# Performance work log

Hardware: AMD Instinct MI355X
Metric: run time of the kernel (lower is better)

Reference implementation:

```python
import jax, jax.numpy as jnp
import numpy as np

L, C, K, V, G, T, NC, CIN = 9, 256, 3, 25, 9, 128, 60, 3


def _ln(x, w, b, axes, eps=1e-5):
    # LayerNorm over (channels, joints) per time step, affine params broadcast over time
    m = x.mean(axes, keepdims=True)
    v = x.var(axes, keepdims=True)
    return (x - m) * jax.lax.rsqrt(v + eps) * w + b


def setup_inputs() -> dict:
    key = jax.random.key(0)
    ks = jax.random.split(key, 8)
    s = 0.02  # weight init scale
    return {
        "x": jax.random.normal(ks[0], (1, CIN, T, V), jnp.float32),
        "A": jax.random.uniform(ks[1], (K, V, V), jnp.float32),
        "ln_in_w": jnp.ones((CIN, V), jnp.float32),
        "ln_in_b": jnp.zeros((CIN, V), jnp.float32),
        "W_in": jax.random.normal(ks[2], (C, CIN), jnp.float32) * s,
        "b_in": jnp.zeros((C,), jnp.float32),
        "Wg": jax.random.normal(ks[3], (L, K * C, C), jnp.float32) * s,
        "bg": jnp.zeros((L, K * C), jnp.float32),
        "ln1_w": jnp.ones((L, C, V), jnp.float32),
        "ln1_b": jnp.zeros((L, C, V), jnp.float32),
        "Wt": jax.random.normal(ks[4], (L, C, C, G), jnp.float32) * s,
        "bt": jnp.zeros((L, C), jnp.float32),
        "ln2_w": jnp.ones((L, C, V), jnp.float32),
        "ln2_b": jnp.zeros((L, C, V), jnp.float32),
        "imp": jnp.ones((L, K, V, V), jnp.float32),
        "W_out": jax.random.normal(ks[5], (NC, C), jnp.float32) * s,
        "b_out": jnp.zeros((NC,), jnp.float32),
    }


def reference(x, A, ln_in_w, ln_in_b, W_in, b_in, Wg, bg, ln1_w, ln1_b,
              Wt, bt, ln2_w, ln2_b, imp, W_out, b_out):
    ghalf = G // 2
    Al = A[None] * imp                      # (L, K, V, V) edge-importance weighted adjacency
    xs = x[0].transpose(1, 0, 2)            # (T, CIN, V): stream frames
    fifo0 = jnp.zeros((L, C, G, V), x.dtype)

    def step(carry, xt):
        fifo, fifo_res = carry
        # input LayerNorm + 1x1 conv (fcn_in)
        h = _ln(xt, ln_in_w, ln_in_b, (0, 1))
        h = jnp.einsum('oc,cv->ov', W_in, h) + b_in[:, None]   # (C, V)
        new_f, new_fr = [], []
        for l in range(L):
            res = h                                             # identity residual (in==out, stride==1)
            # graph conv: 1x1 conv -> (K, C, V), einsum with partitioned adjacency
            y = (jnp.einsum('oc,cv->ov', Wg[l], h) + bg[l][:, None]).reshape(K, C, V)
            z = jnp.einsum('kcv,kvw->cw', y, Al[l])             # (C, V)
            # FIFO shift: newest frame at time index 0
            f = jnp.concatenate([z[:, None, :], fifo[l, :, :-1]], axis=1)      # (C, G, V)
            fr = jnp.concatenate([res[:, None, :], fifo_res[l, :, :-1]], axis=1)
            # tcn: LN -> ReLU -> temporal conv (G,1) -> LN
            a = jax.nn.relu(_ln(f, ln1_w[l][:, None, :], ln1_b[l][:, None, :], (0, 2)))
            t = jnp.einsum('ocg,cgv->ov', Wt[l], a) + bt[l][:, None]           # (C, V)
            t = _ln(t, ln2_w[l], ln2_b[l], (0, 1))
            # residual from center of residual FIFO, then ReLU
            h = jax.nn.relu(t + fr[:, ghalf])
            new_f.append(f)
            new_fr.append(fr)
        pooled = h.mean(axis=1)                                 # avg_pool2d over (T=1, V)
        logits = W_out @ pooled + b_out                         # (NC,)
        return (jnp.stack(new_f), jnp.stack(new_fr)), logits

    _, out = jax.lax.scan(step, (fifo0, fifo0), xs)
    return out  # (T, NC): per-frame class logits
```

## Files before the change

kernel.cpp:

```cpp
#include <hip/hip_runtime.h>

#define TT  128
#define CC  256
#define VV  25
#define KK  3
#define GG  9
#define LL  9
#define NCC 60
#define CINN 3
#define TV    (TT*VV)
#define N4    4096
#define KDIM2 (CC*GG)
#define UR    ((TT+8)*32)
#define KSPLIT 4
#define KCH   (KDIM2/KSPLIT)

typedef __attribute__((ext_vector_type(8))) short bf16x8;
typedef __attribute__((ext_vector_type(4))) float f32x4;
typedef unsigned short us16;

__device__ __forceinline__ us16 f2bf(float f) {
    union { float f; unsigned u; } a; a.f = f;
    unsigned r = a.u + 0x7fff + ((a.u >> 16) & 1);
    return (us16)(r >> 16);
}
__device__ __forceinline__ bf16x8 ld8(const us16* p) { return *(const bf16x8*)p; }


#define PN1 (LL*KK*CC*CC)
#define PN2 (LL*CC*CC*GG)
#define PN3 (LL*KK*32*32)
#define PN4 (LL*CC*32)
#define PTOT (PN1+PN2+PN3+PN4)

__global__ void k_prep(const float* __restrict__ Wg, const float* __restrict__ Wt,
                       const float* __restrict__ A, const float* __restrict__ imp,
                       const float* __restrict__ bg,
                       us16* __restrict__ Wgb, us16* __restrict__ Wt2b,
                       us16* __restrict__ AlTb, float* __restrict__ bgAl) {
    int i = blockIdx.x * 256 + threadIdx.x;
    if (i < PN1) {
        Wgb[i] = f2bf(Wg[i]);
    } else if (i < PN1 + PN2) {
        int j = i - PN1;
        int kk = j % (CC*GG);
        int o  = (j / (CC*GG)) % CC;
        int l  = j / (CC*CC*GG);
        int g = kk >> 8, c = kk & 255;
        Wt2b[j] = f2bf(Wt[((size_t)(l*CC + o)*CC + c)*GG + g]);
    } else if (i < PN1 + PN2 + PN3) {
        int j = i - PN1 - PN2;
        int v = j & 31, w = (j >> 5) & 31;
        int lk = j >> 10, k = lk % KK, l = lk / KK;
        float val = 0.f;
        if (v < VV && w < VV)
            val = A[(k*VV+v)*VV + w] * imp[((size_t)(l*KK+k)*VV+v)*VV + w];
        AlTb[j] = f2bf(val);
    } else if (i < PTOT) {
        int j = i - PN1 - PN2 - PN3;
        int w = j & 31, c = (j >> 5) & 255, l = j >> 13;
        float s = 0.f;
        if (w < VV) {
            for (int k = 0; k < KK; k++) {
                float col = 0.f;
                for (int v = 0; v < VV; v++)
                    col += A[(k*VV+v)*VV + w] * imp[((size_t)(l*KK+k)*VV+v)*VV + w];
                s += bg[l*KK*CC + k*CC + c] * col;
            }
        }
        bgAl[j] = s;
    }
}


__global__ __launch_bounds__(256) void k_h0(const float* __restrict__ x,
                                            const float* __restrict__ lnw,
                                            const float* __restrict__ lnb,
                                            const float* __restrict__ Win,
                                            const float* __restrict__ bin,
                                            float* __restrict__ H,
                                            us16* __restrict__ Hbt2) {
    int t = blockIdx.x, tid = threadIdx.x;
    __shared__ float sx[CINN*VV];
    __shared__ float sh[CINN*VV];
    if (tid < CINN*VV)
        sx[tid] = x[(size_t)(tid/VV)*TV + t*VV + (tid%VV)];
    __syncthreads();
    float s = 0.f, q = 0.f;
    for (int i = 0; i < CINN*VV; i++) { float v = sx[i]; s += v; q += v*v; }
    float m  = s * (1.f/75.f);
    float var = q * (1.f/75.f) - m*m;
    float rs = rsqrtf(var + 1e-5f);
    if (tid < CINN*VV)
        sh[tid] = (sx[tid]-m)*rs*lnw[tid] + lnb[tid];
    __syncthreads();
    int c = tid;
    float w0 = Win[c*3+0], w1 = Win[c*3+1], w2 = Win[c*3+2], b = bin[c];
    #pragma unroll
    for (int v = 0; v < VV; v++) {
        float acc = b + w0*sh[v] + w1*sh[VV+v] + w2*sh[2*VV+v];
        H[(size_t)c*N4 + t*32 + v] = acc;
        Hbt2[(size_t)(t*32 + v)*CC + c] = f2bf(acc);
    }
    #pragma unroll
    for (int v = VV; v < 32; v++)
        Hbt2[(size_t)(t*32 + v)*CC + c] = 0;
}


__device__ __forceinline__ void blk_reduce2(float& s, float& q, float* red) {
    #pragma unroll
    for (int off = 32; off; off >>= 1) {
        s += __shfl_down(s, off);
        q += __shfl_down(q, off);
    }
    int lane = threadIdx.x & 63, w = threadIdx.x >> 6;
    if (lane == 0) { red[w] = s; red[4+w] = q; }
    __syncthreads();
    s = red[0]+red[1]+red[2]+red[3];
    q = red[4]+red[5]+red[6]+red[7];
}


__global__ __launch_bounds__(256) void k_gemm1(const us16* __restrict__ A,
                                               const us16* __restrict__ Bt,
                                               us16* __restrict__ Ybt) {
    __shared__ us16 Yl[64*72];
    const int tid = threadIdx.x;
    const int wave = tid >> 6, lane = tid & 63, quad = lane >> 4, l16 = lane & 15;
    const int m0w = blockIdx.y * 64 + (wave & 1) * 32;
    const int n0w = blockIdx.x * 64 + (wave >> 1) * 32;
    const us16* ap = A + (size_t)(m0w + l16) * CC + quad * 8;
    const us16* bp = Bt + (size_t)(n0w + l16) * CC + quad * 8;
    f32x4 acc[2][2] = {};
    #pragma unroll
    for (int s = 0; s < 8; s++) {
        bf16x8 a0 = ld8(ap + s*32);
        bf16x8 a1 = ld8(ap + s*32 + 16*CC);
        bf16x8 b0 = ld8(bp + s*32);
        bf16x8 b1 = ld8(bp + s*32 + 16*CC);
        acc[0][0] = __builtin_amdgcn_mfma_f32_16x16x32_bf16(a0, b0, acc[0][0], 0,0,0);
        acc[0][1] = __builtin_amdgcn_mfma_f32_16x16x32_bf16(a0, b1, acc[0][1], 0,0,0);
        acc[1][0] = __builtin_amdgcn_mfma_f32_16x16x32_bf16(a1, b0, acc[1][0], 0,0,0);
        acc[1][1] = __builtin_amdgcn_mfma_f32_16x16x32_bf16(a1, b1, acc[1][1], 0,0,0);
    }
    #pragma unroll
    for (int mt = 0; mt < 2; mt++)
        #pragma unroll
        for (int nt = 0; nt < 2; nt++)
            #pragma unroll
            for (int r = 0; r < 4; r++) {
                int m_loc = (wave & 1)*32 + mt*16 + quad*4 + r;
                int n_loc = (wave >> 1)*32 + nt*16 + l16;
                Yl[m_loc*72 + n_loc] = f2bf(acc[mt][nt][r]);
            }
    __syncthreads();
    const int kidx = (blockIdx.y * 64) >> 8;
    const int c0   = (blockIdx.y * 64) & 255;
    const int t0   = blockIdx.x * 2;
    #pragma unroll
    for (int u = 0; u < 2; u++) {
        int q = tid*2 + u;
        int ch = q & 3, row = q >> 2;
        int cl = row & 63, tl = row >> 6;
        bf16x8 val = *(const bf16x8*)(Yl + cl*72 + tl*32 + ch*8);
        *(bf16x8*)(Ybt + ((size_t)((t0+tl)*CC + c0 + cl))*96 + kidx*32 + ch*8) = val;
    }
}


__global__ __launch_bounds__(256) void k_adj(const us16* __restrict__ Ybt,
                                             const us16* __restrict__ AlTb,
                                             const float* __restrict__ bgAl,
                                             const float* __restrict__ lnw,
                                             const float* __restrict__ lnb,
                                             us16* __restrict__ Ut2) {
    int t = blockIdx.x, tid = threadIdx.x;
    if (t >= TT) {
        int tp = t - TT, c = tid;
        #pragma unroll
        for (int w = 0; w < 32; w++) {
            float u = (w < VV) ? fmaxf(lnb[c*VV + w], 0.f) : 0.f;
            Ut2[(size_t)(tp*32 + w)*CC + c] = f2bf(u);
        }
        return;
    }
    __shared__ float red[8];
    const int wave = tid >> 6, lane = tid & 63, quad = lane >> 4, l16 = lane & 15;
    bf16x8 al[2][3];
    #pragma unroll
    for (int nt = 0; nt < 2; nt++)
        #pragma unroll
        for (int s = 0; s < 3; s++)
            al[nt][s] = ld8(AlTb + (size_t)(s*32 + nt*16 + l16)*32 + quad*8);
    f32x4 z[4][2];
    #pragma unroll
    for (int mt = 0; mt < 4; mt++) { z[mt][0] = (f32x4){}; z[mt][1] = (f32x4){}; }
    #pragma unroll
    for (int mt = 0; mt < 4; mt++) {
        const us16* yp = Ybt + ((size_t)(t*CC + wave*64 + mt*16 + l16))*96 + quad*8;
        #pragma unroll
        for (int s = 0; s < 3; s++) {
            bf16x8 a = ld8(yp + s*32);
            z[mt][0] = __builtin_amdgcn_mfma_f32_16x16x32_bf16(a, al[0][s], z[mt][0], 0,0,0);
            z[mt][1] = __builtin_amdgcn_mfma_f32_16x16x32_bf16(a, al[1][s], z[mt][1], 0,0,0);
        }
    }
    float s_ = 0.f, q_ = 0.f;
    #pragma unroll
    for (int mt = 0; mt < 4; mt++)
        #pragma unroll
        for (int nt = 0; nt < 2; nt++)
            #pragma unroll
            for (int r = 0; r < 4; r++) {
                int c = wave*64 + mt*16 + quad*4 + r;
                int w = nt*16 + l16;
                float zb = z[mt][nt][r] + bgAl[c*32 + w];
                z[mt][nt][r] = zb;
                if (w < VV) { s_ += zb; q_ += zb*zb; }
            }
    blk_reduce2(s_, q_, red);
    float m = s_ * (1.f/6400.f);
    float var = q_ * (1.f/6400.f) - m*m;
    float rs = rsqrtf(var + 1e-5f);
    #pragma unroll
    for (int mt = 0; mt < 4; mt++)
        #pragma unroll
        for (int nt = 0; nt < 2; nt++) {
            int w = nt*16 + l16;
            if (w < VV) {
                int c0 = wave*64 + mt*16 + quad*4;
                ushort4 pk;
                float u0 = fmaxf((z[mt][nt][0]-m)*rs*lnw[(c0+0)*VV+w] + lnb[(c0+0)*VV+w], 0.f);
                float u1 = fmaxf((z[mt][nt][1]-m)*rs*lnw[(c0+1)*VV+w] + lnb[(c0+1)*VV+w], 0.f);
                float u2 = fmaxf((z[mt][nt][2]-m)*rs*lnw[(c0+2)*VV+w] + lnb[(c0+2)*VV+w], 0.f);
                float u3 = fmaxf((z[mt][nt][3]-m)*rs*lnw[(c0+3)*VV+w] + lnb[(c0+3)*VV+w], 0.f);
                pk.x = f2bf(u0); pk.y = f2bf(u1); pk.z = f2bf(u2); pk.w = f2bf(u3);
                *(ushort4*)(Ut2 + (size_t)((t+8)*32 + w)*CC + c0) = pk;
            }
        }
    #pragma unroll
    for (int r = VV; r < 32; r++)
        Ut2[(size_t)((t+8)*32 + r)*CC + tid] = 0;
}


__global__ __launch_bounds__(256) void k_gemm2(const us16* __restrict__ A,
                                               const us16* __restrict__ Ut2,
                                               float* __restrict__ TCp) {
    const int tid = threadIdx.x;
    const int wave = tid >> 6, lane = tid & 63, quad = lane >> 4, l16 = lane & 15;
    const int m0w = blockIdx.y * 64 + (wave & 1) * 32;
    const int n0w = blockIdx.x * 64 + (wave >> 1) * 32;
    const int ks = blockIdx.z;
    const int kbeg = ks * KCH, kend = kbeg + KCH;
    float* TC = TCp + (size_t)ks * CC * N4;
    const us16* ap = A + (size_t)(m0w + l16) * KDIM2 + quad * 8;
    f32x4 acc00 = {}, acc01 = {}, acc10 = {}, acc11 = {};
    bf16x8 a0, a1, b0, b1;

    auto loadAB = [&](int k0, bf16x8& x0, bf16x8& x1, bf16x8& y0, bf16x8& y1) {
        x0 = ld8(ap + k0);
        x1 = ld8(ap + k0 + 16*KDIM2);
        int g = k0 >> 8;
        const us16* bp = Ut2 + (size_t)(n0w + (8-g)*32 + l16)*CC + (k0 & 255) + quad*8;
        y0 = ld8(bp);
        y1 = ld8(bp + 16*CC);
    };
    loadAB(kbeg, a0, a1, b0, b1);
    #pragma unroll 3
    for (int k0 = kbeg + 32; k0 < kend; k0 += 32) {
        bf16x8 c0, c1, d0, d1;
        loadAB(k0, c0, c1, d0, d1);
        acc00 = __builtin_amdgcn_mfma_f32_16x16x32_bf16(a0, b0, acc00, 0,0,0);
        acc01 = __builtin_amdgcn_mfma_f32_16x16x32_bf16(a0, b1, acc01, 0,0,0);
        acc10 = __builtin_amdgcn_mfma_f32_16x16x32_bf16(a1, b0, acc10, 0,0,0);
        acc11 = __builtin_amdgcn_mfma_f32_16x16x32_bf16(a1, b1, acc11, 0,0,0);
        a0 = c0; a1 = c1; b0 = d0; b1 = d1;
    }
    acc00 = __builtin_amdgcn_mfma_f32_16x16x32_bf16(a0, b0, acc00, 0,0,0);
    acc01 = __builtin_amdgcn_mfma_f32_16x16x32_bf16(a0, b1, acc01, 0,0,0);
    acc10 = __builtin_amdgcn_mfma_f32_16x16x32_bf16(a1, b0, acc10, 0,0,0);
    acc11 = __builtin_amdgcn_mfma_f32_16x16x32_bf16(a1, b1, acc11, 0,0,0);

    const int r0 = m0w + quad*4;
    const int col = n0w + l16;
    #pragma unroll
    for (int r = 0; r < 4; r++) {
        TC[(size_t)(r0 + r)*N4 + col]           = acc00[r];
        TC[(size_t)(r0 + r)*N4 + col + 16]      = acc01[r];
        TC[(size_t)(r0 + 16 + r)*N4 + col]      = acc10[r];
        TC[(size_t)(r0 + 16 + r)*N4 + col + 16] = acc11[r];
    }
}


__global__ __launch_bounds__(256) void k_ln2(const float* __restrict__ TCp,
                                             const float* __restrict__ bt,
                                             const float* __restrict__ lnw,
                                             const float* __restrict__ lnb,
                                             const float* __restrict__ Hin,
                                             float* __restrict__ Hout,
                                             us16* __restrict__ Hbt2) {
    int t = blockIdx.x, tid = threadIdx.x;
    __shared__ float sv[CC*33];
    __shared__ float red[8];
    #pragma unroll
    for (int j = 0; j < 8; j++) {
        int c = j*32 + (tid >> 3);
        int v4 = (tid & 7) * 4;
        size_t base = (size_t)c*N4 + t*32 + v4;
        float4 x = *(const float4*)(TCp + base);
        #pragma unroll
        for (int s = 1; s < KSPLIT; s++) {
            float4 y = *(const float4*)(TCp + (size_t)s*CC*N4 + base);
            x.x += y.x; x.y += y.y; x.z += y.z; x.w += y.w;
        }
        sv[c*33 + v4+0] = x.x; sv[c*33 + v4+1] = x.y;
        sv[c*33 + v4+2] = x.z; sv[c*33 + v4+3] = x.w;
    }
    __syncthreads();
    int c = tid;
    float btc = bt[c];
    float vals[VV];
    float s = 0.f, q = 0.f;
    #pragma unroll
    for (int v = 0; v < VV; v++) {
        float x = sv[c*33 + v] + btc;
        vals[v] = x; s += x; q += x*x;
    }
    blk_reduce2(s, q, red);
    float m = s * (1.f/6400.f);
    float var = q * (1.f/6400.f) - m*m;
    float rs = rsqrtf(var + 1e-5f);
    #pragma unroll
    for (int v = 0; v < VV; v++) {
        float res = (t >= 4) ? Hin[(size_t)c*N4 + (t-4)*32 + v] : 0.f;
        float o = fmaxf((vals[v]-m)*rs*lnw[c*VV+v] + lnb[c*VV+v] + res, 0.f);
        Hout[(size_t)c*N4 + t*32 + v] = o;
        sv[c*33 + v] = o;
    }
    #pragma unroll
    for (int v = 0; v < VV; v++)
        Hbt2[(size_t)(t*32 + v)*CC + tid] = f2bf(sv[tid*33 + v]);
    #pragma unroll
    for (int v = VV; v < 32; v++)
        Hbt2[(size_t)(t*32 + v)*CC + tid] = 0;
}


__global__ __launch_bounds__(256) void k_out(const float* __restrict__ H,
                                             const float* __restrict__ Wout,
                                             const float* __restrict__ bout,
                                             float* __restrict__ out) {
    int t = blockIdx.x, tid = threadIdx.x;
    __shared__ float sp[CC];
    float s = 0.f;
    for (int v = 0; v < VV; v++) s += H[(size_t)tid*N4 + t*32 + v];
    sp[tid] = s * (1.f/VV);
    __syncthreads();
    if (tid < NCC) {
        float acc = bout[tid];
        for (int c = 0; c < CC; c++) acc = fmaf(Wout[tid*CC+c], sp[c], acc);
        out[t*NCC + tid] = acc;
    }
}


extern "C" void kernel_launch(void* const* d_in, const int* in_sizes, int n_in,
                              void* d_out, int out_size, void* d_ws, size_t ws_size,
                              hipStream_t stream) {
    const float* x    = (const float*)d_in[0];
    const float* A    = (const float*)d_in[1];
    const float* lniw = (const float*)d_in[2];
    const float* lnib = (const float*)d_in[3];
    const float* Win  = (const float*)d_in[4];
    const float* bin  = (const float*)d_in[5];
    const float* Wg   = (const float*)d_in[6];
    const float* bg   = (const float*)d_in[7];
    const float* ln1w = (const float*)d_in[8];
    const float* ln1b = (const float*)d_in[9];
    const float* Wt   = (const float*)d_in[10];
    const float* bt   = (const float*)d_in[11];
    const float* ln2w = (const float*)d_in[12];
    const float* ln2b = (const float*)d_in[13];
    const float* imp  = (const float*)d_in[14];
    const float* Wout = (const float*)d_in[15];
    const float* bout = (const float*)d_in[16];
    float* out = (float*)d_out;

    float* ws = (float*)d_ws;
    size_t off = 0;
    auto alloc = [&](size_t n) { float* p = ws + off; off += (n + 255) & ~(size_t)255; return p; };
    float* H0   = alloc((size_t)CC*N4);
    float* H1   = alloc((size_t)CC*N4);
    float* TCp  = alloc((size_t)KSPLIT*CC*N4);
    float* bgAl = alloc((size_t)LL*CC*32);
    us16* Wgb  = (us16*)alloc((size_t)LL*KK*CC*CC/2);
    us16* Wt2b = (us16*)alloc((size_t)LL*CC*KDIM2/2);
    us16* Hbt2 = (us16*)alloc((size_t)N4*CC/2);
    us16* Ut2  = (us16*)alloc((size_t)UR*CC/2);
    us16* AlTb = (us16*)alloc((size_t)LL*KK*32*32/2);
    us16* Ybt  = (us16*)alloc((size_t)TT*CC*96/2);
    (void)ws_size; (void)in_sizes; (void)n_in; (void)out_size;

    k_prep<<<(PTOT + 255)/256, 256, 0, stream>>>(Wg, Wt, A, imp, bg,
                                                 Wgb, Wt2b, AlTb, bgAl);
    k_h0<<<TT, 256, 0, stream>>>(x, lniw, lnib, Win, bin, H0, Hbt2);

    float* Hin = H0; float* Hout = H1;
    for (int l = 0; l < LL; l++) {
        k_gemm1<<<dim3(N4/64, (KK*CC)/64), 256, 0, stream>>>(
            Wgb + (size_t)l*KK*CC*CC, Hbt2, Ybt);
        k_adj<<<TT + 8, 256, 0, stream>>>(
            Ybt, AlTb + (size_t)l*KK*32*32, bgAl + (size_t)l*CC*32,
            ln1w + l*CC*VV, ln1b + l*CC*VV, Ut2);
        k_gemm2<<<dim3(N4/64, CC/64, KSPLIT), 256, 0, stream>>>(
            Wt2b + (size_t)l*CC*KDIM2, Ut2, TCp);
        k_ln2<<<TT, 256, 0, stream>>>(
            TCp, bt + l*CC, ln2w + l*CC*VV, ln2b + l*CC*VV, Hin, Hout, Hbt2);
        float* tmp = Hin; Hin = Hout; Hout = tmp;
    }
    k_out<<<TT, 256, 0, stream>>>(Hin, Wout, bout, out);
}
```

Baseline: 880.2 us.

## Fuse LN2/residual into next layer's GEMM1, drop split-K in GEMM2

Removes the separate k_ln2 kernel. Each k_gemm1 block (except layer 0) now recomputes the LayerNorm, residual add and ReLU for its two frames from the full-K GEMM2 output and stages the bf16 result in LDS as the B operand. The final layer's LN2 is folded into k_out. GEMM2 drops its 4-way split-K and uses a two-deep register prefetch instead. H is stored transposed (time-major) for coalesced residual reads. The trade-off is that all 12 row-blocks redundantly recompute the LN for their frames, and GEMM2 has 4x fewer blocks, which lowers its parallelism.

```diff
diff --git a/kernel.cpp b/kernel.cpp
--- a/kernel.cpp
+++ b/kernel.cpp
@@ -12,8 +12,8 @@
 #define N4    4096
 #define KDIM2 (CC*GG)
 #define UR    ((TT+8)*32)
-#define KSPLIT 4
-#define KCH   (KDIM2/KSPLIT)
+#define BSTR  264
+#define FSTR  33
 
 typedef __attribute__((ext_vector_type(8))) short bf16x8;
 typedef __attribute__((ext_vector_type(4))) float f32x4;
@@ -78,7 +78,7 @@
                                             const float* __restrict__ lnb,
                                             const float* __restrict__ Win,
                                             const float* __restrict__ bin,
-                                            float* __restrict__ H,
+                                            float* __restrict__ HT,
                                             us16* __restrict__ Hbt2) {
     int t = blockIdx.x, tid = threadIdx.x;
     __shared__ float sx[CINN*VV];
@@ -99,7 +99,7 @@
     #pragma unroll
     for (int v = 0; v < VV; v++) {
         float acc = b + w0*sh[v] + w1*sh[VV+v] + w2*sh[2*VV+v];
-        H[(size_t)c*N4 + t*32 + v] = acc;
+        HT[(size_t)(t*32 + v)*CC + c] = acc;
         Hbt2[(size_t)(t*32 + v)*CC + c] = f2bf(acc);
     }
     #pragma unroll
@@ -122,28 +122,97 @@
 }
 
 
+template<int FLN>
 __global__ __launch_bounds__(256) void k_gemm1(const us16* __restrict__ A,
                                                const us16* __restrict__ Bt,
+                                               const float* __restrict__ TC,
+                                               const float* __restrict__ HprevT,
+                                               const float* __restrict__ lnw,
+                                               const float* __restrict__ lnb,
+                                               const float* __restrict__ btv,
+                                               float* __restrict__ HnextT,
                                                us16* __restrict__ Ybt) {
-    __shared__ us16 Yl[64*72];
+    __shared__ __align__(16) float sF[CC*FSTR];
+    __shared__ __align__(16) us16 sB[64*BSTR];
+    __shared__ float red[8];
     const int tid = threadIdx.x;
     const int wave = tid >> 6, lane = tid & 63, quad = lane >> 4, l16 = lane & 15;
-    const int m0w = blockIdx.y * 64 + (wave & 1) * 32;
-    const int n0w = blockIdx.x * 64 + (wave >> 1) * 32;
-    const us16* ap = A + (size_t)(m0w + l16) * CC + quad * 8;
-    const us16* bp = Bt + (size_t)(n0w + l16) * CC + quad * 8;
+    const int bx = blockIdx.x, by = blockIdx.y;
+
+    if (FLN) {
+        const int t0 = bx*2;
+        const int c = tid;
+        const float btc = btv[c];
+        #pragma unroll
+        for (int f = 0; f < 2; f++) {
+            const int t = t0 + f;
+            #pragma unroll
+            for (int j = 0; j < 8; j++) {
+                int cs = j*32 + (tid >> 3);
+                int v4 = (tid & 7) * 4;
+                float4 xv = *(const float4*)(TC + (size_t)cs*N4 + t*32 + v4);
+                sF[cs*FSTR + v4+0] = xv.x; sF[cs*FSTR + v4+1] = xv.y;
+                sF[cs*FSTR + v4+2] = xv.z; sF[cs*FSTR + v4+3] = xv.w;
+            }
+            __syncthreads();
+            float vals[VV];
+            float s = 0.f, q = 0.f;
+            #pragma unroll
+            for (int v = 0; v < VV; v++) {
+                float xv = sF[c*FSTR + v] + btc;
+                vals[v] = xv; s += xv; q += xv*xv;
+            }
+            blk_reduce2(s, q, red);
+            float m = s * (1.f/6400.f);
+            float var = q * (1.f/6400.f) - m*m;
+            float rs = rsqrtf(var + 1e-5f);
+            #pragma unroll
+            for (int v = 0; v < VV; v++) {
+                float res = (t >= 4) ? HprevT[(size_t)((t-4)*32 + v)*CC + c] : 0.f;
+                float o = fmaxf((vals[v]-m)*rs*lnw[c*VV+v] + lnb[c*VV+v] + res, 0.f);
+                if (by == 0) HnextT[(size_t)(t*32 + v)*CC + c] = o;
+                sB[(f*32 + v)*BSTR + c] = f2bf(o);
+            }
+            #pragma unroll
+            for (int v = VV; v < 32; v++)
+                sB[(f*32 + v)*BSTR + c] = 0;
+            __syncthreads();
+        }
+    }
+
+    const int m0w = by*64 + (wave & 1)*32;
+    const us16* ap = A + (size_t)(m0w + l16)*CC + quad*8;
     f32x4 acc[2][2] = {};
-    #pragma unroll
-    for (int s = 0; s < 8; s++) {
-        bf16x8 a0 = ld8(ap + s*32);
-        bf16x8 a1 = ld8(ap + s*32 + 16*CC);
-        bf16x8 b0 = ld8(bp + s*32);
-        bf16x8 b1 = ld8(bp + s*32 + 16*CC);
-        acc[0][0] = __builtin_amdgcn_mfma_f32_16x16x32_bf16(a0, b0, acc[0][0], 0,0,0);
-        acc[0][1] = __builtin_amdgcn_mfma_f32_16x16x32_bf16(a0, b1, acc[0][1], 0,0,0);
-        acc[1][0] = __builtin_amdgcn_mfma_f32_16x16x32_bf16(a1, b0, acc[1][0], 0,0,0);
-        acc[1][1] = __builtin_amdgcn_mfma_f32_16x16x32_bf16(a1, b1, acc[1][1], 0,0,0);
-    }
+    if (FLN) {
+        const int nl = (wave >> 1)*32 + l16;
+        #pragma unroll
+        for (int s = 0; s < 8; s++) {
+            bf16x8 a0 = ld8(ap + s*32);
+            bf16x8 a1 = ld8(ap + s*32 + 16*CC);
+            bf16x8 b0 = *(const bf16x8*)(sB + (size_t)nl*BSTR + s*32 + quad*8);
+            bf16x8 b1 = *(const bf16x8*)(sB + (size_t)(nl+16)*BSTR + s*32 + quad*8);
+            acc[0][0] = __builtin_amdgcn_mfma_f32_16x16x32_bf16(a0, b0, acc[0][0], 0,0,0);
+            acc[0][1] = __builtin_amdgcn_mfma_f32_16x16x32_bf16(a0, b1, acc[0][1], 0,0,0);
+            acc[1][0] = __builtin_amdgcn_mfma_f32_16x16x32_bf16(a1, b0, acc[1][0], 0,0,0);
+            acc[1][1] = __builtin_amdgcn_mfma_f32_16x16x32_bf16(a1, b1, acc[1][1], 0,0,0);
+        }
+    } else {
+        const int n0w = bx*64 + (wave >> 1)*32;
+        const us16* bp = Bt + (size_t)(n0w + l16)*CC + quad*8;
+        #pragma unroll
+        for (int s = 0; s < 8; s++) {
+            bf16x8 a0 = ld8(ap + s*32);
+            bf16x8 a1 = ld8(ap + s*32 + 16*CC);
+            bf16x8 b0 = ld8(bp + s*32);
+            bf16x8 b1 = ld8(bp + s*32 + 16*CC);
+            acc[0][0] = __builtin_amdgcn_mfma_f32_16x16x32_bf16(a0, b0, acc[0][0], 0,0,0);
+            acc[0][1] = __builtin_amdgcn_mfma_f32_16x16x32_bf16(a0, b1, acc[0][1], 0,0,0);
+            acc[1][0] = __builtin_amdgcn_mfma_f32_16x16x32_bf16(a1, b0, acc[1][0], 0,0,0);
+            acc[1][1] = __builtin_amdgcn_mfma_f32_16x16x32_bf16(a1, b1, acc[1][1], 0,0,0);
+        }
+    }
+    __syncthreads();
+    us16* Yl = (us16*)sF;
     #pragma unroll
     for (int mt = 0; mt < 2; mt++)
         #pragma unroll
@@ -155,16 +224,16 @@
                 Yl[m_loc*72 + n_loc] = f2bf(acc[mt][nt][r]);
             }
     __syncthreads();
-    const int kidx = (blockIdx.y * 64) >> 8;
-    const int c0   = (blockIdx.y * 64) & 255;
-    const int t0   = blockIdx.x * 2;
+    const int kidx = (by*64) >> 8;
+    const int c0   = (by*64) & 255;
+    const int t0s  = bx*2;
     #pragma unroll
     for (int u = 0; u < 2; u++) {
-        int q = tid*2 + u;
-        int ch = q & 3, row = q >> 2;
+        int qq = tid*2 + u;
+        int ch = qq & 3, row = qq >> 2;
         int cl = row & 63, tl = row >> 6;
         bf16x8 val = *(const bf16x8*)(Yl + cl*72 + tl*32 + ch*8);
-        *(bf16x8*)(Ybt + ((size_t)((t0+tl)*CC + c0 + cl))*96 + kidx*32 + ch*8) = val;
+        *(bf16x8*)(Ybt + ((size_t)((t0s+tl)*CC + c0 + cl))*96 + kidx*32 + ch*8) = val;
     }
 }
 
@@ -247,17 +316,14 @@
 
 __global__ __launch_bounds__(256) void k_gemm2(const us16* __restrict__ A,
                                                const us16* __restrict__ Ut2,
-                                               float* __restrict__ TCp) {
+                                               float* __restrict__ TC) {
     const int tid = threadIdx.x;
     const int wave = tid >> 6, lane = tid & 63, quad = lane >> 4, l16 = lane & 15;
     const int m0w = blockIdx.y * 64 + (wave & 1) * 32;
     const int n0w = blockIdx.x * 64 + (wave >> 1) * 32;
-    const int ks = blockIdx.z;
-    const int kbeg = ks * KCH, kend = kbeg + KCH;
-    float* TC = TCp + (size_t)ks * CC * N4;
     const us16* ap = A + (size_t)(m0w + l16) * KDIM2 + quad * 8;
     f32x4 acc00 = {}, acc01 = {}, acc10 = {}, acc11 = {};
-    bf16x8 a0, a1, b0, b1;
+    bf16x8 a0[2], a1[2], b0[2], b1[2];
 
     auto loadAB = [&](int k0, bf16x8& x0, bf16x8& x1, bf16x8& y0, bf16x8& y1) {
         x0 = ld8(ap + k0);
@@ -267,21 +333,24 @@
         y0 = ld8(bp);
         y1 = ld8(bp + 16*CC);
     };
-    loadAB(kbeg, a0, a1, b0, b1);
-    #pragma unroll 3
-    for (int k0 = kbeg + 32; k0 < kend; k0 += 32) {
-        bf16x8 c0, c1, d0, d1;
-        loadAB(k0, c0, c1, d0, d1);
-        acc00 = __builtin_amdgcn_mfma_f32_16x16x32_bf16(a0, b0, acc00, 0,0,0);
-        acc01 = __builtin_amdgcn_mfma_f32_16x16x32_bf16(a0, b1, acc01, 0,0,0);
-        acc10 = __builtin_amdgcn_mfma_f32_16x16x32_bf16(a1, b0, acc10, 0,0,0);
-        acc11 = __builtin_amdgcn_mfma_f32_16x16x32_bf16(a1, b1, acc11, 0,0,0);
-        a0 = c0; a1 = c1; b0 = d0; b1 = d1;
-    }
-    acc00 = __builtin_amdgcn_mfma_f32_16x16x32_bf16(a0, b0, acc00, 0,0,0);
-    acc01 = __builtin_amdgcn_mfma_f32_16x16x32_bf16(a0, b1, acc01, 0,0,0);
-    acc10 = __builtin_amdgcn_mfma_f32_16x16x32_bf16(a1, b0, acc10, 0,0,0);
-    acc11 = __builtin_amdgcn_mfma_f32_16x16x32_bf16(a1, b1, acc11, 0,0,0);
+    auto domfma = [&](bf16x8 x0, bf16x8 x1, bf16x8 y0, bf16x8 y1) {
+        acc00 = __builtin_amdgcn_mfma_f32_16x16x32_bf16(x0, y0, acc00, 0,0,0);
+        acc01 = __builtin_amdgcn_mfma_f32_16x16x32_bf16(x0, y1, acc01, 0,0,0);
+        acc10 = __builtin_amdgcn_mfma_f32_16x16x32_bf16(x1, y0, acc10, 0,0,0);
+        acc11 = __builtin_amdgcn_mfma_f32_16x16x32_bf16(x1, y1, acc11, 0,0,0);
+    };
+
+    loadAB(0,  a0[0], a1[0], b0[0], b1[0]);
+    loadAB(32, a0[1], a1[1], b0[1], b1[1]);
+    #pragma unroll 2
+    for (int k0 = 64; k0 < KDIM2; k0 += 32) {
+        int sl = (k0 >> 5) & 1;
+        bf16x8 ta0 = a0[sl], ta1 = a1[sl], tb0 = b0[sl], tb1 = b1[sl];
+        loadAB(k0, a0[sl], a1[sl], b0[sl], b1[sl]);
+        domfma(ta0, ta1, tb0, tb1);
+    }
+    domfma(a0[0], a1[0], b0[0], b1[0]);
+    domfma(a0[1], a1[1], b0[1], b1[1]);
 
     const int r0 = m0w + quad*4;
     const int col = n0w + l16;
@@ -295,73 +364,52 @@
 }
 
 
-__global__ __launch_bounds__(256) void k_ln2(const float* __restrict__ TCp,
-                                             const float* __restrict__ bt,
+__global__ __launch_bounds__(256) void k_out(const float* __restrict__ TC,
+                                             const float* __restrict__ HT,
+                                             const float* __restrict__ btv,
                                              const float* __restrict__ lnw,
                                              const float* __restrict__ lnb,
-                                             const float* __restrict__ Hin,
-                                             float* __restrict__ Hout,
-                                             us16* __restrict__ Hbt2) {
+                                             const float* __restrict__ Wout,
+                                             const float* __restrict__ bout,
+                                             float* __restrict__ out) {
     int t = blockIdx.x, tid = threadIdx.x;
-    __shared__ float sv[CC*33];
+    __shared__ float sF[CC*FSTR];
     __shared__ float red[8];
+    __shared__ float sp[CC];
     #pragma unroll
     for (int j = 0; j < 8; j++) {
-        int c = j*32 + (tid >> 3);
+        int cs = j*32 + (tid >> 3);
         int v4 = (tid & 7) * 4;
-        size_t base = (size_t)c*N4 + t*32 + v4;
-        float4 x = *(const float4*)(TCp + base);
-        #pragma unroll
-        for (int s = 1; s < KSPLIT; s++) {
-            float4 y = *(const float4*)(TCp + (size_t)s*CC*N4 + base);
-            x.x += y.x; x.y += y.y; x.z += y.z; x.w += y.w;
-        }
-        sv[c*33 + v4+0] = x.x; sv[c*33 + v4+1] = x.y;
-        sv[c*33 + v4+2] = x.z; sv[c*33 + v4+3] = x.w;
+        float4 xv = *(const float4*)(TC + (size_t)cs*N4 + t*32 + v4);
+        sF[cs*FSTR + v4+0] = xv.x; sF[cs*FSTR + v4+1] = xv.y;
+        sF[cs*FSTR + v4+2] = xv.z; sF[cs*FSTR + v4+3] = xv.w;
     }
     __syncthreads();
     int c = tid;
-    float btc = bt[c];
+    float btc = btv[c];
     float vals[VV];
     float s = 0.f, q = 0.f;
     #pragma unroll
     for (int v = 0; v < VV; v++) {
-        float x = sv[c*33 + v] + btc;
-        vals[v] = x; s += x; q += x*x;
+        float xv = sF[c*FSTR + v] + btc;
+        vals[v] = xv; s += xv; q += xv*xv;
     }
     blk_reduce2(s, q, red);
     float m = s * (1.f/6400.f);
     float var = q * (1.f/6400.f) - m*m;
     float rs = rsqrtf(var + 1e-5f);
+    float pool = 0.f;
     #pragma unroll
     for (int v = 0; v < VV; v++) {
-        float res = (t >= 4) ? Hin[(size_t)c*N4 + (t-4)*32 + v] : 0.f;
+        float res = (t >= 4) ? HT[(size_t)((t-4)*32 + v)*CC + c] : 0.f;
         float o = fmaxf((vals[v]-m)*rs*lnw[c*VV+v] + lnb[c*VV+v] + res, 0.f);
-        Hout[(size_t)c*N4 + t*32 + v] = o;
-        sv[c*33 + v] = o;
-    }
-    #pragma unroll
-    for (int v = 0; v < VV; v++)
-        Hbt2[(size_t)(t*32 + v)*CC + tid] = f2bf(sv[tid*33 + v]);
-    #pragma unroll
-    for (int v = VV; v < 32; v++)
-        Hbt2[(size_t)(t*32 + v)*CC + tid] = 0;
-}
-
-
-__global__ __launch_bounds__(256) void k_out(const float* __restrict__ H,
-                                             const float* __restrict__ Wout,
-                                             const float* __restrict__ bout,
-                                             float* __restrict__ out) {
-    int t = blockIdx.x, tid = threadIdx.x;
-    __shared__ float sp[CC];
-    float s = 0.f;
-    for (int v = 0; v < VV; v++) s += H[(size_t)tid*N4 + t*32 + v];
-    sp[tid] = s * (1.f/VV);
+        pool += o;
+    }
+    sp[c] = pool * (1.f/VV);
     __syncthreads();
     if (tid < NCC) {
         float acc = bout[tid];
-        for (int c = 0; c < CC; c++) acc = fmaf(Wout[tid*CC+c], sp[c], acc);
+        for (int cc = 0; cc < CC; cc++) acc = fmaf(Wout[tid*CC+cc], sp[cc], acc);
         out[t*NCC + tid] = acc;
     }
 }
@@ -392,9 +440,9 @@
     float* ws = (float*)d_ws;
     size_t off = 0;
     auto alloc = [&](size_t n) { float* p = ws + off; off += (n + 255) & ~(size_t)255; return p; };
-    float* H0   = alloc((size_t)CC*N4);
-    float* H1   = alloc((size_t)CC*N4);
-    float* TCp  = alloc((size_t)KSPLIT*CC*N4);
+    float* H0   = alloc((size_t)N4*CC);
+    float* H1   = alloc((size_t)N4*CC);
+    float* TC   = alloc((size_t)CC*N4);
     float* bgAl = alloc((size_t)LL*CC*32);
     us16* Wgb  = (us16*)alloc((size_t)LL*KK*CC*CC/2);
     us16* Wt2b = (us16*)alloc((size_t)LL*CC*KDIM2/2);
@@ -408,18 +456,25 @@
                                                  Wgb, Wt2b, AlTb, bgAl);
     k_h0<<<TT, 256, 0, stream>>>(x, lniw, lnib, Win, bin, H0, Hbt2);
 
-    float* Hin = H0; float* Hout = H1;
+    float* hPrev = H0; float* hNext = H1;
     for (int l = 0; l < LL; l++) {
-        k_gemm1<<<dim3(N4/64, (KK*CC)/64), 256, 0, stream>>>(
-            Wgb + (size_t)l*KK*CC*CC, Hbt2, Ybt);
+        if (l == 0) {
+            k_gemm1<0><<<dim3(64, 12), 256, 0, stream>>>(
+                Wgb, Hbt2, TC, hPrev, ln2w, ln2b, bt, hNext, Ybt);
+        } else {
+            k_gemm1<1><<<dim3(64, 12), 256, 0, stream>>>(
+                Wgb + (size_t)l*KK*CC*CC, Hbt2, TC, hPrev,
+                ln2w + (size_t)(l-1)*CC*VV, ln2b + (size_t)(l-1)*CC*VV,
+                bt + (size_t)(l-1)*CC, hNext, Ybt);
+            float* tmp = hPrev; hPrev = hNext; hNext = tmp;
+        }
         k_adj<<<TT + 8, 256, 0, stream>>>(
             Ybt, AlTb + (size_t)l*KK*32*32, bgAl + (size_t)l*CC*32,
-            ln1w + l*CC*VV, ln1b + l*CC*VV, Ut2);
-        k_gemm2<<<dim3(N4/64, CC/64, KSPLIT), 256, 0, stream>>>(
-            Wt2b + (size_t)l*CC*KDIM2, Ut2, TCp);
-        k_ln2<<<TT, 256, 0, stream>>>(
-            TCp, bt + l*CC, ln2w + l*CC*VV, ln2b + l*CC*VV, Hin, Hout, Hbt2);
-        float* tmp = Hin; Hin = Hout; Hout = tmp;
-    }
-    k_out<<<TT, 256, 0, stream>>>(Hin, Wout, bout, out);
-}
+            ln1w + (size_t)l*CC*VV, ln1b + (size_t)l*CC*VV, Ut2);
+        k_gemm2<<<dim3(N4/64, CC/64), 256, 0, stream>>>(
+            Wt2b + (size_t)l*CC*KDIM2, Ut2, TC);
+    }
+    k_out<<<TT, 256, 0, stream>>>(TC, hPrev,
+        bt + (size_t)(LL-1)*CC, ln2w + (size_t)(LL-1)*CC*VV, ln2b + (size_t)(LL-1)*CC*VV,
+        Wout, bout, out);
+}
```

Result: slower. 1.128 ms (+28.2%).
